# Kernel optimization log

Measured on AMD Instinct MI355X. Metric: run time of the kernel, lower is better.

Reference implementation:

```python
import jax, jax.numpy as jnp
import numpy as np

NUM_TOKENS = 14
DIM = 128
B, N = 8, 128
NUM_ROUNDS = 5


def setup_inputs() -> dict:
    key = jax.random.key(0)
    ks = jax.random.split(key, 10)
    s = 1.0 / np.sqrt(DIM)
    return {
        "tok": jax.random.randint(ks[0], (B, N), 0, NUM_TOKENS),
        "A": jax.random.uniform(ks[1], (B, N, N), dtype=jnp.float32),
        "embed": jax.random.normal(ks[2], (NUM_TOKENS, DIM), dtype=jnp.float32),
        "W1": jax.random.normal(ks[3], (DIM, 2 * DIM), dtype=jnp.float32) * s,
        "b1": jax.random.normal(ks[4], (DIM,), dtype=jnp.float32) * s,
        "W2": jax.random.normal(ks[5], (DIM, DIM), dtype=jnp.float32) * s,
        "b2": jax.random.normal(ks[6], (DIM,), dtype=jnp.float32) * s,
        "Wo1": jax.random.normal(ks[7], (DIM, DIM), dtype=jnp.float32) * s,
        "bo1": jax.random.normal(ks[8], (DIM,), dtype=jnp.float32) * s,
        "Wo2": jax.random.normal(ks[9], (10, DIM), dtype=jnp.float32) * s,
    }


def reference(tok, A, embed, W1, b1, W2, b2, Wo1, bo1, Wo2):
    # Dropout is identity (eval mode / inference reference).
    x = embed[tok]  # [B, N, D]
    d = x.shape[-1]
    # fc1 on concat(x_i, x_j) decomposes into two per-node projections:
    # fc1([x_i, x_j]) = x_i @ W1a^T + x_j @ W1b^T + b1
    W1a, W1b = W1[:, :d], W1[:, d:]
    A_t = jnp.swapaxes(A, 1, 2)  # A.transpose(1, 2)
    for _ in range(NUM_ROUNDS):
        hi = jnp.einsum("bnd,ed->bne", x, W1a)
        hj = jnp.einsum("bnd,ed->bne", x, W1b)
        # pairwise edge MLP: [B, N, N, D]
        h = jax.nn.relu(hi[:, :, None, :] + hj[:, None, :, :] + b1)
        m = jax.nn.relu(jnp.einsum("bijd,ed->bije", h, W2) + b2)
        # mask by transposed adjacency and sum over neighbors j (axis 2)
        msg = jnp.einsum("bij,bije->bie", A_t, m)
        x = x + msg
    def head(z):
        return jax.nn.relu(z @ Wo1.T + bo1) @ Wo2.T
    out = head(x[:, 0, :])                       # [B, 10]
    x_all = head(x.reshape(-1, d)).reshape(x.shape[0], x.shape[1], 10)
    return (out, x_all)
```

## Files before the change

kernel.cpp:

```cpp
#include <hip/hip_runtime.h>
#include <hip/hip_bf16.h>

#define NN 128
#define DD 128

typedef __attribute__((ext_vector_type(8))) short bf16x8;
typedef __attribute__((ext_vector_type(4))) float floatx4;
typedef __attribute__((ext_vector_type(2))) float floatx2;

__device__ __forceinline__ unsigned short f2bf_hw(float f) {
    unsigned int r;
    asm("v_cvt_pk_bf16_f32 %0, %1, %2" : "=v"(r) : "v"(f), "v"(f));
    return (unsigned short)r;
}

__device__ __forceinline__ unsigned int f2bf_pk(float lo, float hi) {
    unsigned int r;
    asm("v_cvt_pk_bf16_f32 %0, %1, %2" : "=v"(r) : "v"(lo), "v"(hi));
    return r;
}

#define WS_HJB0 0
#define WS_HJB1 65536
#define WS_CNT  131072

__global__ __launch_bounds__(256) void k_init(float* __restrict__ ws) {
    int* cnt = (int*)(ws + WS_CNT);
    int t = threadIdx.x;
#pragma unroll
    for (int it = 0; it < 5; ++it) cnt[it * 256 + t] = 0;
}

__global__ __launch_bounds__(512, 2) void k_main(const int* __restrict__ tokp,
                                                 const float* __restrict__ embf,
                                                 const float* __restrict__ Af,
                                                 const float* __restrict__ W1f,
                                                 const float* __restrict__ b1f,
                                                 const float* __restrict__ W2f,
                                                 const float* __restrict__ b2f,
                                                 const float* __restrict__ Wo1f,
                                                 const float* __restrict__ bo1f,
                                                 const float* __restrict__ Wo2f,
                                                 float* __restrict__ ws,
                                                 float* __restrict__ outp) {
    __shared__ __align__(16) unsigned short xo[4 * 136];
    __shared__ __align__(16) float red[4][4][128];
    __shared__ __align__(16) float zs[4][128];
    __shared__ float a_s[4][128];
    __shared__ __align__(16) float hja_s[4][128];
    __shared__ __align__(16) float hjb_s[4][128];

    int* cnt = (int*)(ws + WS_CNT);

    int blk = blockIdx.x;
    int b = blk & 7, g = blk >> 3, i0 = g * 4;
    int t = threadIdx.x;
    int wave = t >> 6, lane = t & 63;
    int col = lane & 15, quad = lane >> 4;
    int we = wave & 1, wj = wave >> 1;
    int ebase = we * 64, jbase = wj * 32;

    union U4 { bf16x8 v; unsigned int u[4]; };

    bf16x8 bw[4][4];
#pragma unroll
    for (int et = 0; et < 4; ++et)
#pragma unroll
        for (int ks = 0; ks < 4; ++ks) {
            const float* p = W2f + (ebase + et * 16 + col) * 128 + ks * 32 + quad * 8;
            float4 lo = *reinterpret_cast<const float4*>(p);
            float4 hi = *reinterpret_cast<const float4*>(p + 4);
            U4 w;
            w.u[0] = f2bf_pk(lo.x, lo.y); w.u[1] = f2bf_pk(lo.z, lo.w);
            w.u[2] = f2bf_pk(hi.x, hi.y); w.u[3] = f2bf_pk(hi.z, hi.w);
            bw[et][ks] = w.v;
        }
    bf16x8 w1fr[2][4];
#pragma unroll
    for (int u = 0; u < 2; ++u)
#pragma unroll
        for (int ks = 0; ks < 4; ++ks) {
            int n = (wave * 2 + u) * 16 + col;
            const float* p = W1f + (n & 127) * 256 + (n >> 7) * 128 + ks * 32 + quad * 8;
            float4 lo = *reinterpret_cast<const float4*>(p);
            float4 hi = *reinterpret_cast<const float4*>(p + 4);
            U4 w;
            w.u[0] = f2bf_pk(lo.x, lo.y); w.u[1] = f2bf_pk(lo.z, lo.w);
            w.u[2] = f2bf_pk(hi.x, hi.y); w.u[3] = f2bf_pk(hi.z, hi.w);
            w1fr[u][ks] = w.v;
        }

    float b1r[2];
    b1r[0] = (wave >= 4) ? b1f[((wave - 4) * 2 + 0) * 16 + col] : 0.f;
    b1r[1] = (wave >= 4) ? b1f[((wave - 4) * 2 + 1) * 16 + col] : 0.f;
    float b2r[4];
#pragma unroll
    for (int et = 0; et < 4; ++et) b2r[et] = b2f[ebase + et * 16 + col];

    int ii_own = t >> 7, e_own = t & 127;
    a_s[ii_own][e_own] = Af[(b * NN + e_own) * NN + i0 + ii_own];
    int trow = tokp[b * NN + i0 + ii_own];
    float xown = embf[trow * DD + e_own];
    xo[ii_own * 136 + e_own] = f2bf_hw(xown);
    __syncthreads();

    for (int r = 0; r < 5; ++r) {
        unsigned short* gbw = (unsigned short*)(ws + ((r & 1) ? WS_HJB1 : WS_HJB0));

        {
            bf16x8 af[4];
#pragma unroll
            for (int ks = 0; ks < 4; ++ks) {
                bf16x8 z = {0, 0, 0, 0, 0, 0, 0, 0};
                af[ks] = (col < 4) ? *reinterpret_cast<const bf16x8*>(&xo[col * 136 + ks * 32 + quad * 8]) : z;
            }
            floatx4 acc0 = (floatx4){0.f, 0.f, 0.f, 0.f};
            floatx4 acc1 = (floatx4){0.f, 0.f, 0.f, 0.f};
#pragma unroll
            for (int ks = 0; ks < 4; ++ks) {
                acc0 = __builtin_amdgcn_mfma_f32_16x16x32_bf16(af[ks], w1fr[0][ks], acc0, 0, 0, 0);
                acc1 = __builtin_amdgcn_mfma_f32_16x16x32_bf16(af[ks], w1fr[1][ks], acc1, 0, 0, 0);
            }
            if (quad == 0) {
                if (wave < 4) {
#pragma unroll
                    for (int rr = 0; rr < 4; ++rr) {
                        hja_s[rr][(wave * 2 + 0) * 16 + col] = acc0[rr];
                        hja_s[rr][(wave * 2 + 1) * 16 + col] = acc1[rr];
                    }
                } else {
#pragma unroll
                    for (int rr = 0; rr < 4; ++rr) {
                        hjb_s[rr][((wave - 4) * 2 + 0) * 16 + col] = acc0[rr] + b1r[0];
                        hjb_s[rr][((wave - 4) * 2 + 1) * 16 + col] = acc1[rr] + b1r[1];
                    }
                }
            }
        }
        __syncthreads();
        if (!(e_own & 1)) {
            unsigned int pk = f2bf_pk(hjb_s[ii_own][e_own], hjb_s[ii_own][e_own + 1]);
            int row = b * NN + i0 + ii_own;
            __hip_atomic_store((unsigned int*)gbw + row * 64 + (e_own >> 1), pk,
                               __ATOMIC_RELAXED, __HIP_MEMORY_SCOPE_AGENT);
        }
        __builtin_amdgcn_s_waitcnt(0);
        __syncthreads();
        if (t == 0) {
            int* myc = cnt + (b * 5 + r) * 32;
            __hip_atomic_fetch_add(myc, 1, __ATOMIC_RELAXED, __HIP_MEMORY_SCOPE_AGENT);
            while (__hip_atomic_load(myc, __ATOMIC_RELAXED, __HIP_MEMORY_SCOPE_AGENT) < 32)
                __builtin_amdgcn_s_sleep(1);
        }
        __syncthreads();

        U4 L[2][4];
        {
            const unsigned short* base0 = gbw + (size_t)(b * NN + jbase + col) * 128 + quad * 8;
            const unsigned short* base1 = gbw + (size_t)(b * NN + jbase + 16 + col) * 128 + quad * 8;
            asm volatile(
                "global_load_dwordx4 %0, %8, off sc0 sc1\n\t"
                "global_load_dwordx4 %1, %8, off offset:64 sc0 sc1\n\t"
                "global_load_dwordx4 %2, %8, off offset:128 sc0 sc1\n\t"
                "global_load_dwordx4 %3, %8, off offset:192 sc0 sc1\n\t"
                "global_load_dwordx4 %4, %9, off sc0 sc1\n\t"
                "global_load_dwordx4 %5, %9, off offset:64 sc0 sc1\n\t"
                "global_load_dwordx4 %6, %9, off offset:128 sc0 sc1\n\t"
                "global_load_dwordx4 %7, %9, off offset:192 sc0 sc1"
                : "=&v"(L[0][0].v), "=&v"(L[0][1].v), "=&v"(L[0][2].v), "=&v"(L[0][3].v),
                  "=&v"(L[1][0].v), "=&v"(L[1][1].v), "=&v"(L[1][2].v), "=&v"(L[1][3].v)
                : "v"(base0), "v"(base1)
                : "memory");
        }
        asm volatile("s_waitcnt vmcnt(0)" ::: "memory");
        __builtin_amdgcn_sched_barrier(0);

#pragma unroll
        for (int ii = 0; ii < 4; ++ii) {
            floatx4 acc2[2][4];
#pragma unroll
            for (int jt = 0; jt < 2; ++jt)
#pragma unroll
                for (int et = 0; et < 4; ++et) acc2[jt][et] = (floatx4){0.f, 0.f, 0.f, 0.f};
#pragma unroll
            for (int ks = 0; ks < 4; ++ks) {
                int k0 = ks * 32 + quad * 8;
#pragma unroll
                for (int jt = 0; jt < 2; ++jt) {
                    U4 Ho;
#pragma unroll
                    for (int p = 0; p < 4; ++p) {
                        floatx2 hj, ha2, s2;
                        hj.x = __uint_as_float(L[jt][ks].u[p] << 16);
                        hj.y = __uint_as_float(L[jt][ks].u[p] & 0xFFFF0000u);
                        ha2 = *reinterpret_cast<const floatx2*>(&hja_s[ii][k0 + 2 * p]);
                        asm("v_pk_add_f32 %0, %1, %2" : "=v"(s2) : "v"(hj), "v"(ha2));
                        Ho.u[p] = f2bf_pk(fmaxf(s2.x, 0.f), fmaxf(s2.y, 0.f));
                    }
#pragma unroll
                    for (int et = 0; et < 4; ++et)
                        acc2[jt][et] = __builtin_amdgcn_mfma_f32_16x16x32_bf16(Ho.v, bw[et][ks], acc2[jt][et], 0, 0, 0);
                }
            }
#pragma unroll
            for (int et = 0; et < 4; ++et) {
                float be = b2r[et];
                float s = 0.f;
#pragma unroll
                for (int jt = 0; jt < 2; ++jt) {
                    int j0 = jbase + jt * 16 + quad * 4;
#pragma unroll
                    for (int rr = 0; rr < 4; ++rr)
                        s += a_s[ii][j0 + rr] * fmaxf(acc2[jt][et][rr] + be, 0.f);
                }
                s += __shfl_xor(s, 16, 64);
                s += __shfl_xor(s, 32, 64);
                if (quad == 0) red[wj][ii][ebase + et * 16 + col] = s;
            }
        }
        __syncthreads();
        {
            float msg = red[0][ii_own][e_own] + red[1][ii_own][e_own]
                      + red[2][ii_own][e_own] + red[3][ii_own][e_own];
            xown += msg;
            if (r < 4) xo[ii_own * 136 + e_own] = f2bf_hw(xown);
            else       zs[ii_own][e_own] = xown;
        }
        __syncthreads();
    }

    {
        const float4* wrow = reinterpret_cast<const float4*>(Wo1f + e_own * 128);
        float acc = 0.f;
#pragma unroll
        for (int d4 = 0; d4 < 32; ++d4) {
            float4 w = wrow[d4];
            float4 z = *reinterpret_cast<const float4*>(&zs[ii_own][d4 * 4]);
            acc += w.x * z.x + w.y * z.y + w.z * z.z + w.w * z.w;
        }
        ((float*)red)[ii_own * 128 + e_own] = fmaxf(acc + bo1f[e_own], 0.f);
    }
    __syncthreads();
    if (t < 40) {
        int ii = t / 10, o = t - ii * 10;
        const float* rsrow = (const float*)red + ii * 128;
        const float4* w2r = reinterpret_cast<const float4*>(Wo2f + o * DD);
        float s = 0.f;
#pragma unroll
        for (int e4 = 0; e4 < 32; ++e4) {
            float4 rv = *reinterpret_cast<const float4*>(&rsrow[e4 * 4]);
            float4 wv = w2r[e4];
            s += rv.x * wv.x + rv.y * wv.y + rv.z * wv.z + rv.w * wv.w;
        }
        int row = b * NN + i0 + ii;
        outp[80 + row * 10 + o] = s;
        if (i0 + ii == 0) outp[b * 10 + o] = s;
    }
}

extern "C" void kernel_launch(void* const* d_in, const int* in_sizes, int n_in,
                              void* d_out, int out_size, void* d_ws, size_t ws_size,
                              hipStream_t stream) {
    const int*   tok  = (const int*)d_in[0];
    const float* Af   = (const float*)d_in[1];
    const float* embf = (const float*)d_in[2];
    const float* W1f  = (const float*)d_in[3];
    const float* b1f  = (const float*)d_in[4];
    const float* W2f  = (const float*)d_in[5];
    const float* b2f  = (const float*)d_in[6];
    const float* Wo1f = (const float*)d_in[7];
    const float* bo1f = (const float*)d_in[8];
    const float* Wo2f = (const float*)d_in[9];

    float* ws  = (float*)d_ws;
    float* out = (float*)d_out;

    k_init<<<1, 256, 0, stream>>>(ws);
    k_main<<<256, 512, 0, stream>>>(tok, embf, Af, W1f, b1f, W2f, b2f, Wo1f, bo1f, Wo2f, ws, out);
}
```

Before: 141.9 us.

## Skip round-0 grid barrier via per-token projection table; use per-block flags

In round 0 every node embedding is one of 14 token vectors, so each block now computes the W1a/W1b projections for all 14 tokens into shared-memory tables. It then gathers its hi/hj values from those tables instead of publishing hj to global memory and waiting on the inter-block barrier. For later rounds the counter-based barrier becomes per-block flag stores that one wave polls with a wave-wide vote. This removes one global sync and its round trip, at the cost of a little redundant MFMA work per block and extra LDS.

```diff
diff --git a/kernel.cpp b/kernel.cpp
--- a/kernel.cpp
+++ b/kernel.cpp
@@ -22,13 +22,11 @@
 
 #define WS_HJB0 0
 #define WS_HJB1 65536
-#define WS_CNT  131072
+#define WS_FLG  131072
 
 __global__ __launch_bounds__(256) void k_init(float* __restrict__ ws) {
-    int* cnt = (int*)(ws + WS_CNT);
-    int t = threadIdx.x;
-#pragma unroll
-    for (int it = 0; it < 5; ++it) cnt[it * 256 + t] = 0;
+    int* fl = (int*)(ws + WS_FLG);
+    if (threadIdx.x < 256) fl[threadIdx.x] = 0;
 }
 
 __global__ __launch_bounds__(512, 2) void k_main(const int* __restrict__ tokp,
@@ -49,8 +47,11 @@
     __shared__ float a_s[4][128];
     __shared__ __align__(16) float hja_s[4][128];
     __shared__ __align__(16) float hjb_s[4][128];
-
-    int* cnt = (int*)(ws + WS_CNT);
+    __shared__ __align__(16) float tabA[14 * 128];
+    __shared__ __align__(16) unsigned short tabB[14 * 128];
+    __shared__ int tokj[128];
+
+    int* flg = (int*)(ws + WS_FLG);
 
     int blk = blockIdx.x;
     int b = blk & 7, g = blk >> 3, i0 = g * 4;
@@ -99,81 +100,142 @@
 
     int ii_own = t >> 7, e_own = t & 127;
     a_s[ii_own][e_own] = Af[(b * NN + e_own) * NN + i0 + ii_own];
+    if (t < 128) tokj[t] = tokp[b * NN + t];
     int trow = tokp[b * NN + i0 + ii_own];
     float xown = embf[trow * DD + e_own];
-    xo[ii_own * 136 + e_own] = f2bf_hw(xown);
+
+    {
+        bf16x8 afT[4];
+#pragma unroll
+        for (int ks = 0; ks < 4; ++ks) {
+            bf16x8 z = {0, 0, 0, 0, 0, 0, 0, 0};
+            if (col < 14) {
+                const float* p = embf + col * 128 + ks * 32 + quad * 8;
+                float4 lo = *reinterpret_cast<const float4*>(p);
+                float4 hi = *reinterpret_cast<const float4*>(p + 4);
+                U4 w;
+                w.u[0] = f2bf_pk(lo.x, lo.y); w.u[1] = f2bf_pk(lo.z, lo.w);
+                w.u[2] = f2bf_pk(hi.x, hi.y); w.u[3] = f2bf_pk(hi.z, hi.w);
+                afT[ks] = w.v;
+            } else afT[ks] = z;
+        }
+        floatx4 ta0 = (floatx4){0.f, 0.f, 0.f, 0.f};
+        floatx4 ta1 = (floatx4){0.f, 0.f, 0.f, 0.f};
+#pragma unroll
+        for (int ks = 0; ks < 4; ++ks) {
+            ta0 = __builtin_amdgcn_mfma_f32_16x16x32_bf16(afT[ks], w1fr[0][ks], ta0, 0, 0, 0);
+            ta1 = __builtin_amdgcn_mfma_f32_16x16x32_bf16(afT[ks], w1fr[1][ks], ta1, 0, 0, 0);
+        }
+        if (wave < 4) {
+            int n0 = (wave * 2 + 0) * 16 + col, n1 = (wave * 2 + 1) * 16 + col;
+#pragma unroll
+            for (int rr = 0; rr < 4; ++rr) {
+                int v = quad * 4 + rr;
+                if (v < 14) { tabA[v * 128 + n0] = ta0[rr]; tabA[v * 128 + n1] = ta1[rr]; }
+            }
+        } else {
+            int d0 = ((wave - 4) * 2 + 0) * 16 + col, d1 = ((wave - 4) * 2 + 1) * 16 + col;
+#pragma unroll
+            for (int rr = 0; rr < 4; ++rr) {
+                float v0 = ta0[rr] + b1r[0]; float p0 = __shfl_xor(v0, 1, 64);
+                float v1 = ta1[rr] + b1r[1]; float p1 = __shfl_xor(v1, 1, 64);
+                int v = quad * 4 + rr;
+                if (!(col & 1) && v < 14) {
+                    ((unsigned int*)tabB)[v * 64 + (d0 >> 1)] = f2bf_pk(v0, p0);
+                    ((unsigned int*)tabB)[v * 64 + (d1 >> 1)] = f2bf_pk(v1, p1);
+                }
+            }
+        }
+    }
     __syncthreads();
 
     for (int r = 0; r < 5; ++r) {
         unsigned short* gbw = (unsigned short*)(ws + ((r & 1) ? WS_HJB1 : WS_HJB0));
-
-        {
-            bf16x8 af[4];
+        U4 L[2][4];
+
+        if (r == 0) {
+            hja_s[ii_own][e_own] = tabA[trow * 128 + e_own];
+            __syncthreads();
+            int tv0 = tokj[jbase + col], tv1 = tokj[jbase + 16 + col];
 #pragma unroll
             for (int ks = 0; ks < 4; ++ks) {
-                bf16x8 z = {0, 0, 0, 0, 0, 0, 0, 0};
-                af[ks] = (col < 4) ? *reinterpret_cast<const bf16x8*>(&xo[col * 136 + ks * 32 + quad * 8]) : z;
-            }
-            floatx4 acc0 = (floatx4){0.f, 0.f, 0.f, 0.f};
-            floatx4 acc1 = (floatx4){0.f, 0.f, 0.f, 0.f};
-#pragma unroll
-            for (int ks = 0; ks < 4; ++ks) {
-                acc0 = __builtin_amdgcn_mfma_f32_16x16x32_bf16(af[ks], w1fr[0][ks], acc0, 0, 0, 0);
-                acc1 = __builtin_amdgcn_mfma_f32_16x16x32_bf16(af[ks], w1fr[1][ks], acc1, 0, 0, 0);
-            }
-            if (quad == 0) {
-                if (wave < 4) {
-#pragma unroll
-                    for (int rr = 0; rr < 4; ++rr) {
-                        hja_s[rr][(wave * 2 + 0) * 16 + col] = acc0[rr];
-                        hja_s[rr][(wave * 2 + 1) * 16 + col] = acc1[rr];
+                L[0][ks].v = *reinterpret_cast<const bf16x8*>(&tabB[tv0 * 128 + ks * 32 + quad * 8]);
+                L[1][ks].v = *reinterpret_cast<const bf16x8*>(&tabB[tv1 * 128 + ks * 32 + quad * 8]);
+            }
+        } else {
+            {
+                bf16x8 af[4];
+#pragma unroll
+                for (int ks = 0; ks < 4; ++ks) {
+                    bf16x8 z = {0, 0, 0, 0, 0, 0, 0, 0};
+                    af[ks] = (col < 4) ? *reinterpret_cast<const bf16x8*>(&xo[col * 136 + ks * 32 + quad * 8]) : z;
+                }
+                floatx4 acc0 = (floatx4){0.f, 0.f, 0.f, 0.f};
+                floatx4 acc1 = (floatx4){0.f, 0.f, 0.f, 0.f};
+#pragma unroll
+                for (int ks = 0; ks < 4; ++ks) {
+                    acc0 = __builtin_amdgcn_mfma_f32_16x16x32_bf16(af[ks], w1fr[0][ks], acc0, 0, 0, 0);
+                    acc1 = __builtin_amdgcn_mfma_f32_16x16x32_bf16(af[ks], w1fr[1][ks], acc1, 0, 0, 0);
+                }
+                if (quad == 0) {
+                    if (wave < 4) {
+#pragma unroll
+                        for (int rr = 0; rr < 4; ++rr) {
+                            hja_s[rr][(wave * 2 + 0) * 16 + col] = acc0[rr];
+                            hja_s[rr][(wave * 2 + 1) * 16 + col] = acc1[rr];
+                        }
+                    } else {
+#pragma unroll
+                        for (int rr = 0; rr < 4; ++rr) {
+                            hjb_s[rr][((wave - 4) * 2 + 0) * 16 + col] = acc0[rr] + b1r[0];
+                            hjb_s[rr][((wave - 4) * 2 + 1) * 16 + col] = acc1[rr] + b1r[1];
+                        }
                     }
-                } else {
-#pragma unroll
-                    for (int rr = 0; rr < 4; ++rr) {
-                        hjb_s[rr][((wave - 4) * 2 + 0) * 16 + col] = acc0[rr] + b1r[0];
-                        hjb_s[rr][((wave - 4) * 2 + 1) * 16 + col] = acc1[rr] + b1r[1];
+                }
+            }
+            __syncthreads();
+            if (!(e_own & 1)) {
+                unsigned int pk = f2bf_pk(hjb_s[ii_own][e_own], hjb_s[ii_own][e_own + 1]);
+                int row = b * NN + i0 + ii_own;
+                __hip_atomic_store((unsigned int*)gbw + row * 64 + (e_own >> 1), pk,
+                                   __ATOMIC_RELAXED, __HIP_MEMORY_SCOPE_AGENT);
+            }
+            __builtin_amdgcn_s_waitcnt(0);
+            __syncthreads();
+            {
+                int* fl = flg + b * 32;
+                if (t == g)
+                    __hip_atomic_store(fl + g, r, __ATOMIC_RELAXED, __HIP_MEMORY_SCOPE_AGENT);
+                if (t < 64) {
+                    while (true) {
+                        int v = (t < 32) ? __hip_atomic_load(fl + t, __ATOMIC_RELAXED,
+                                                             __HIP_MEMORY_SCOPE_AGENT) : r;
+                        if (__all(v >= r)) break;
+                        __builtin_amdgcn_s_sleep(1);
                     }
                 }
-            }
-        }
-        __syncthreads();
-        if (!(e_own & 1)) {
-            unsigned int pk = f2bf_pk(hjb_s[ii_own][e_own], hjb_s[ii_own][e_own + 1]);
-            int row = b * NN + i0 + ii_own;
-            __hip_atomic_store((unsigned int*)gbw + row * 64 + (e_own >> 1), pk,
-                               __ATOMIC_RELAXED, __HIP_MEMORY_SCOPE_AGENT);
-        }
-        __builtin_amdgcn_s_waitcnt(0);
-        __syncthreads();
-        if (t == 0) {
-            int* myc = cnt + (b * 5 + r) * 32;
-            __hip_atomic_fetch_add(myc, 1, __ATOMIC_RELAXED, __HIP_MEMORY_SCOPE_AGENT);
-            while (__hip_atomic_load(myc, __ATOMIC_RELAXED, __HIP_MEMORY_SCOPE_AGENT) < 32)
-                __builtin_amdgcn_s_sleep(1);
-        }
-        __syncthreads();
-
-        U4 L[2][4];
-        {
-            const unsigned short* base0 = gbw + (size_t)(b * NN + jbase + col) * 128 + quad * 8;
-            const unsigned short* base1 = gbw + (size_t)(b * NN + jbase + 16 + col) * 128 + quad * 8;
-            asm volatile(
-                "global_load_dwordx4 %0, %8, off sc0 sc1\n\t"
-                "global_load_dwordx4 %1, %8, off offset:64 sc0 sc1\n\t"
-                "global_load_dwordx4 %2, %8, off offset:128 sc0 sc1\n\t"
-                "global_load_dwordx4 %3, %8, off offset:192 sc0 sc1\n\t"
-                "global_load_dwordx4 %4, %9, off sc0 sc1\n\t"
-                "global_load_dwordx4 %5, %9, off offset:64 sc0 sc1\n\t"
-                "global_load_dwordx4 %6, %9, off offset:128 sc0 sc1\n\t"
-                "global_load_dwordx4 %7, %9, off offset:192 sc0 sc1"
-                : "=&v"(L[0][0].v), "=&v"(L[0][1].v), "=&v"(L[0][2].v), "=&v"(L[0][3].v),
-                  "=&v"(L[1][0].v), "=&v"(L[1][1].v), "=&v"(L[1][2].v), "=&v"(L[1][3].v)
-                : "v"(base0), "v"(base1)
-                : "memory");
-        }
-        asm volatile("s_waitcnt vmcnt(0)" ::: "memory");
-        __builtin_amdgcn_sched_barrier(0);
+                __syncthreads();
+            }
+            {
+                const unsigned short* base0 = gbw + (size_t)(b * NN + jbase + col) * 128 + quad * 8;
+                const unsigned short* base1 = gbw + (size_t)(b * NN + jbase + 16 + col) * 128 + quad * 8;
+                asm volatile(
+                    "global_load_dwordx4 %0, %8, off sc0 sc1\n\t"
+                    "global_load_dwordx4 %1, %8, off offset:64 sc0 sc1\n\t"
+                    "global_load_dwordx4 %2, %8, off offset:128 sc0 sc1\n\t"
+                    "global_load_dwordx4 %3, %8, off offset:192 sc0 sc1\n\t"
+                    "global_load_dwordx4 %4, %9, off sc0 sc1\n\t"
+                    "global_load_dwordx4 %5, %9, off offset:64 sc0 sc1\n\t"
+                    "global_load_dwordx4 %6, %9, off offset:128 sc0 sc1\n\t"
+                    "global_load_dwordx4 %7, %9, off offset:192 sc0 sc1"
+                    : "=&v"(L[0][0].v), "=&v"(L[0][1].v), "=&v"(L[0][2].v), "=&v"(L[0][3].v),
+                      "=&v"(L[1][0].v), "=&v"(L[1][1].v), "=&v"(L[1][2].v), "=&v"(L[1][3].v)
+                    : "v"(base0), "v"(base1)
+                    : "memory");
+                asm volatile("s_waitcnt vmcnt(0)" ::: "memory");
+                __builtin_amdgcn_sched_barrier(0);
+            }
+        }
 
 #pragma unroll
         for (int ii = 0; ii < 4; ++ii) {
```

Result: no change. 141.8 us (-0.1%).
